# Performance work log

Measured on AMD Instinct MI355X. Metric: run time of the kernel, lower is better.

The kernel has to match this reference:

```python
import jax, jax.numpy as jnp
import numpy as np

# Llama-3-8B-style attention config (from init_kwargs)
DIM = 4096
N_HEADS = 32
N_KV_HEADS = 8
HEAD_DIM = DIM // N_HEADS          # 128
N_REP = N_HEADS // N_KV_HEADS      # 4 (GQA replication)
ROPE_THETA = 10000.0
W_SCALE = 0.02


def setup_inputs() -> dict:
    key = jax.random.key(0)
    kx, kq, kk, kv, ko = jax.random.split(key, 5)
    bsz, seqlen = 1, 2048
    x = jax.random.normal(kx, (bsz, seqlen, DIM), dtype=jnp.float32)
    # nn.Linear(in, out, bias=False) -> store as [in, out] so y = x @ W
    wq = jax.random.normal(kq, (DIM, N_HEADS * HEAD_DIM), dtype=jnp.float32) * W_SCALE
    wk = jax.random.normal(kk, (DIM, N_KV_HEADS * HEAD_DIM), dtype=jnp.float32) * W_SCALE
    wv = jax.random.normal(kv, (DIM, N_KV_HEADS * HEAD_DIM), dtype=jnp.float32) * W_SCALE
    wo = jax.random.normal(ko, (N_HEADS * HEAD_DIM, DIM), dtype=jnp.float32) * W_SCALE
    return {"x": x, "wq": wq, "wk": wk, "wv": wv, "wo": wo, "start_pos": 0}


def _rope_cos_sin(seqlen: int):
    # precompute_freqs_cis: freqs[j] = theta^(-2j/dim), angles = outer(t, freqs)
    inv_freq = 1.0 / (ROPE_THETA ** (jnp.arange(0, HEAD_DIM, 2, dtype=jnp.float32) / HEAD_DIM))
    angles = jnp.arange(seqlen, dtype=jnp.float32)[:, None] * inv_freq[None, :]  # [s, hd/2]
    return jnp.cos(angles), jnp.sin(angles)


def _apply_rope(t, cos, sin):
    # t: [b, s, h, hd]; pairs (even, odd) form complex numbers, rotate by angle
    tr, ti = t[..., 0::2], t[..., 1::2]
    c = cos[None, :, None, :]
    s = sin[None, :, None, :]
    out = jnp.stack([tr * c - ti * s, tr * s + ti * c], axis=-1)  # [b,s,h,hd/2,2]
    return out.reshape(t.shape)


def reference(x, wq, wk, wv, wo, start_pos):
    bsz, seqlen, _ = x.shape
    xq = (x @ wq).reshape(bsz, seqlen, N_HEADS, HEAD_DIM)
    xk = (x @ wk).reshape(bsz, seqlen, N_KV_HEADS, HEAD_DIM)
    xv = (x @ wv).reshape(bsz, seqlen, N_KV_HEADS, HEAD_DIM)

    cos, sin = _rope_cos_sin(seqlen)
    xq = _apply_rope(xq, cos, sin)
    xk = _apply_rope(xk, cos, sin)

    # GQA: repeat_interleave KV heads to match query heads
    xk = jnp.repeat(xk, N_REP, axis=2)
    xv = jnp.repeat(xv, N_REP, axis=2)

    scale = 1.0 / jnp.sqrt(jnp.float32(HEAD_DIM))
    scores = jnp.einsum('bqhd,bkhd->bhqk', xq, xk) * scale  # [b,h,s,s]
    causal = jnp.tril(jnp.ones((seqlen, seqlen), dtype=bool))
    scores = jnp.where(causal[None, None], scores, -jnp.inf)
    probs = jax.nn.softmax(scores, axis=-1)

    out = jnp.einsum('bhqk,bkhd->bqhd', probs, xv)
    out = out.reshape(bsz, seqlen, N_HEADS * HEAD_DIM)
    return out @ wo
```

## Files before the change

kernel.cpp:

```cpp
#include <hip/hip_runtime.h>
#include <stdint.h>

typedef __attribute__((ext_vector_type(8))) short bf16x8;
typedef __attribute__((ext_vector_type(4))) short bf16x4;
typedef __attribute__((ext_vector_type(4))) float f32x4;
typedef __attribute__((ext_vector_type(4))) unsigned short u16x4;

#define DIM   4096
#define SEQ   2048
#define NH    32
#define NKV   8
#define HD    128
#define QKV_N 6144
#define ATT_SCALE 0.08838834764831845f

static __device__ __forceinline__ unsigned short f2bf_bits(float f) {
  uint32_t x = __builtin_bit_cast(uint32_t, f);
  x += 0x7fffu + ((x >> 16) & 1u);
  return (unsigned short)(x >> 16);
}
static __device__ __forceinline__ float bf_bits2f(unsigned short u) {
  uint32_t x = ((uint32_t)u) << 16;
  return __builtin_bit_cast(float, x);
}

__global__ __launch_bounds__(256) void transpose_f32_bf16(
    const float* __restrict__ in, unsigned short* __restrict__ out,
    int ld_in, int ld_out) {
  __shared__ unsigned short sh[32][33];
  const int c0 = blockIdx.x * 32, r0 = blockIdx.y * 32;
  const int t = threadIdx.x;
  const int cc = t & 31, rr = (t >> 5) * 4;
#pragma unroll
  for (int p = 0; p < 4; ++p)
    sh[cc][rr + p] = f2bf_bits(in[(size_t)(r0 + rr + p) * ld_in + (c0 + cc)]);
  __syncthreads();
#pragma unroll
  for (int p = 0; p < 4; ++p)
    out[(size_t)(c0 + rr + p) * ld_out + (r0 + cc)] = sh[rr + p][cc];
}

__global__ __launch_bounds__(256) void transpose_bf16(
    const unsigned short* __restrict__ in, unsigned short* __restrict__ out,
    int ld_in, int ld_out) {
  __shared__ unsigned short sh[32][33];
  const int c0 = blockIdx.x * 32, r0 = blockIdx.y * 32;
  const int t = threadIdx.x;
  const int cc = t & 31, rr = (t >> 5) * 4;
#pragma unroll
  for (int p = 0; p < 4; ++p)
    sh[cc][rr + p] = in[(size_t)(r0 + rr + p) * ld_in + (c0 + cc)];
  __syncthreads();
#pragma unroll
  for (int p = 0; p < 4; ++p)
    out[(size_t)(c0 + rr + p) * ld_out + (r0 + cc)] = sh[rr + p][cc];
}

__global__ __launch_bounds__(256) void convert_f32_bf16(
    const float* __restrict__ in, unsigned short* __restrict__ out) {
  const int i = (blockIdx.x * 256 + threadIdx.x) * 4;
  const float4 v = *(const float4*)&in[i];
  u16x4 w;
  w[0] = f2bf_bits(v.x); w[1] = f2bf_bits(v.y);
  w[2] = f2bf_bits(v.z); w[3] = f2bf_bits(v.w);
  *(u16x4*)&out[i] = w;
}

#define BM 128
#define BN 128
#define BK 32
#define LDSS 40

template <bool OUT_FP32>
__global__ __launch_bounds__(256) void gemm_bt(
    const unsigned short* __restrict__ A, int lda,
    const unsigned short* __restrict__ Bt, int ldb,
    void* __restrict__ C_, int ldc, int K) {
  __shared__ __align__(16) unsigned short ldsA[BM * LDSS];
  __shared__ __align__(16) unsigned short ldsB[BN * LDSS];
  const int t = threadIdx.x;
  const int wave = t >> 6, lane = t & 63;
  const int lane16 = lane & 15, quad = lane >> 4;
  const int m0 = blockIdx.y * BM, n0 = blockIdx.x * BN;
  const int wrow = (wave >> 1) * 64, wcol = (wave & 1) * 64;

  f32x4 acc[4][4];
#pragma unroll
  for (int i = 0; i < 4; ++i)
#pragma unroll
    for (int j = 0; j < 4; ++j) acc[i][j] = (f32x4){0.f, 0.f, 0.f, 0.f};

  const int sr = t >> 2;
  const int sc = (t & 3) * 8;

  for (int kk = 0; kk < K; kk += BK) {
    __syncthreads();
#pragma unroll
    for (int i = 0; i < 2; ++i) {
      const int r = sr + i * 64;
      *(bf16x8*)&ldsA[r * LDSS + sc] =
          *(const bf16x8*)&A[(size_t)(m0 + r) * lda + kk + sc];
      *(bf16x8*)&ldsB[r * LDSS + sc] =
          *(const bf16x8*)&Bt[(size_t)(n0 + r) * ldb + kk + sc];
    }
    __syncthreads();

    bf16x8 af[4], bfr[4];
#pragma unroll
    for (int mi = 0; mi < 4; ++mi)
      af[mi] = *(const bf16x8*)&ldsA[(wrow + mi * 16 + lane16) * LDSS + quad * 8];
#pragma unroll
    for (int ni = 0; ni < 4; ++ni)
      bfr[ni] = *(const bf16x8*)&ldsB[(wcol + ni * 16 + lane16) * LDSS + quad * 8];
#pragma unroll
    for (int mi = 0; mi < 4; ++mi)
#pragma unroll
      for (int ni = 0; ni < 4; ++ni)
        acc[mi][ni] = __builtin_amdgcn_mfma_f32_16x16x32_bf16(
            af[mi], bfr[ni], acc[mi][ni], 0, 0, 0);
  }

#pragma unroll
  for (int mi = 0; mi < 4; ++mi)
#pragma unroll
    for (int ni = 0; ni < 4; ++ni)
#pragma unroll
      for (int r = 0; r < 4; ++r) {
        const int row = m0 + wrow + mi * 16 + quad * 4 + r;
        const int col = n0 + wcol + ni * 16 + lane16;
        if (OUT_FP32)
          ((float*)C_)[(size_t)row * ldc + col] = acc[mi][ni][r];
        else
          ((unsigned short*)C_)[(size_t)row * ldc + col] = f2bf_bits(acc[mi][ni][r]);
      }
}

__global__ __launch_bounds__(256) void rope_kernel(unsigned short* __restrict__ qkv) {
  const int idx = blockIdx.x * 256 + threadIdx.x;
  const int pos = idx / 2560;
  const int rem = idx - pos * 2560;
  const int head = rem >> 6;
  const int i = rem & 63;
  const float inv_freq = __expf(-(float)(2 * i) * (9.210340371976184f / 128.0f));
  const float ang = (float)pos * inv_freq;
  float s, c;
  __sincosf(ang, &s, &c);
  const int col = (head < 32) ? head * 128 + 2 * i
                              : 4096 + (head - 32) * 128 + 2 * i;
  unsigned short* p = qkv + (size_t)pos * QKV_N + col;
  const float tr = bf_bits2f(p[0]), ti = bf_bits2f(p[1]);
  p[0] = f2bf_bits(tr * c - ti * s);
  p[1] = f2bf_bits(tr * s + ti * c);
}

#define QT 64
#define KT 64
#define KLS (HD + 8)
#define VLS (KT + 8)

__global__ __launch_bounds__(256) void attn_kernel(
    const unsigned short* __restrict__ qkv,
    const unsigned short* __restrict__ vT,
    unsigned short* __restrict__ attn) {
  __shared__ __align__(16) unsigned short kls[KT][KLS];
  __shared__ __align__(16) unsigned short vls[HD][VLS];

  const int t = threadIdx.x;
  const int wave = t >> 6, lane = t & 63;
  const int lane16 = lane & 15, quad = lane >> 4;
  const int h = blockIdx.y, kvh = h >> 2;
  const int qt = (gridDim.x - 1) - blockIdx.x;
  const int q0 = qt * QT;
  const int wq0 = q0 + wave * 16;
  const int qrow = wq0 + lane16;

  const unsigned short* qbase = qkv + (size_t)wq0 * QKV_N + h * HD;
  const unsigned short* kbase = qkv + 4096 + kvh * HD;
  const unsigned short* vbase = vT + (size_t)kvh * HD * SEQ;

  bf16x8 qf[4];
#pragma unroll
  for (int dc = 0; dc < 4; ++dc)
    qf[dc] = *(const bf16x8*)&qbase[(size_t)lane16 * QKV_N + dc * 32 + quad * 8];

  f32x4 o[8];
#pragma unroll
  for (int i = 0; i < 8; ++i) o[i] = (f32x4){0.f, 0.f, 0.f, 0.f};
  float m = -INFINITY, l = 0.f;

  const int nkb = qt + 1;
  for (int kb = 0; kb < nkb; ++kb) {
    const int key0 = kb * KT;
    __syncthreads();
    {
      const int r = t >> 2, c = (t & 3) * 8;
      const unsigned short* src = &kbase[(size_t)(key0 + r) * QKV_N];
#pragma unroll
      for (int j = 0; j < 4; ++j)
        *(bf16x8*)&kls[r][c + j * 32] = *(const bf16x8*)&src[c + j * 32];
    }
    {
      const int d = t >> 1, s0 = (t & 1) * 32;
      const unsigned short* src = &vbase[(size_t)d * SEQ + key0];
#pragma unroll
      for (int j = 0; j < 4; ++j)
        *(bf16x8*)&vls[d][s0 + j * 8] = *(const bf16x8*)&src[s0 + j * 8];
    }
    __syncthreads();

    f32x4 S[4];
#pragma unroll
    for (int kt = 0; kt < 4; ++kt) {
      f32x4 sacc = (f32x4){0.f, 0.f, 0.f, 0.f};
#pragma unroll
      for (int dc = 0; dc < 4; ++dc) {
        const bf16x8 kf = *(const bf16x8*)&kls[kt * 16 + lane16][dc * 32 + quad * 8];
        sacc = __builtin_amdgcn_mfma_f32_16x16x32_bf16(kf, qf[dc], sacc, 0, 0, 0);
      }
      S[kt] = sacc;
    }

    float sv[4][4], mx = -INFINITY;
#pragma unroll
    for (int kt = 0; kt < 4; ++kt)
#pragma unroll
      for (int r = 0; r < 4; ++r) {
        const int key = key0 + kt * 16 + quad * 4 + r;
        sv[kt][r] = (key <= qrow) ? S[kt][r] * ATT_SCALE : -INFINITY;
        mx = fmaxf(mx, sv[kt][r]);
      }
    mx = fmaxf(mx, __shfl_xor(mx, 16, 64));
    mx = fmaxf(mx, __shfl_xor(mx, 32, 64));
    const float newm = fmaxf(m, mx);
    const float alpha = __expf(m - newm);
    m = newm;
    float p[4][4], rs = 0.f;
#pragma unroll
    for (int kt = 0; kt < 4; ++kt)
#pragma unroll
      for (int r = 0; r < 4; ++r) {
        p[kt][r] = __expf(sv[kt][r] - newm);
        rs += p[kt][r];
      }
    rs += __shfl_xor(rs, 16, 64);
    rs += __shfl_xor(rs, 32, 64);
    l = l * alpha + rs;
#pragma unroll
    for (int dt = 0; dt < 8; ++dt)
#pragma unroll
      for (int r = 0; r < 4; ++r) o[dt][r] *= alpha;

    bf16x4 pb[4];
#pragma unroll
    for (int kt = 0; kt < 4; ++kt) {
      bf16x4 w;
      w[0] = (short)f2bf_bits(p[kt][0]); w[1] = (short)f2bf_bits(p[kt][1]);
      w[2] = (short)f2bf_bits(p[kt][2]); w[3] = (short)f2bf_bits(p[kt][3]);
      pb[kt] = w;
    }

#pragma unroll
    for (int dt = 0; dt < 8; ++dt)
#pragma unroll
      for (int kt = 0; kt < 4; ++kt) {
        const bf16x4 vf = *(const bf16x4*)&vls[dt * 16 + lane16][kt * 16 + quad * 4];
        o[dt] = __builtin_amdgcn_mfma_f32_16x16x16bf16_1k(vf, pb[kt], o[dt], 0, 0, 0);
      }
  }

  const float inv_l = 1.0f / l;
  unsigned short* dst = attn + (size_t)qrow * DIM + h * HD;
#pragma unroll
  for (int dt = 0; dt < 8; ++dt) {
    u16x4 w;
#pragma unroll
    for (int r = 0; r < 4; ++r) w[r] = f2bf_bits(o[dt][r] * inv_l);
    *(u16x4*)&dst[dt * 16 + quad * 4] = w;
  }
}

extern "C" void kernel_launch(void* const* d_in, const int* in_sizes, int n_in,
                              void* d_out, int out_size, void* d_ws, size_t ws_size,
                              hipStream_t stream) {
  const float* x  = (const float*)d_in[0];
  const float* wq = (const float*)d_in[1];
  const float* wk = (const float*)d_in[2];
  const float* wv = (const float*)d_in[3];
  const float* wo = (const float*)d_in[4];
  float* out = (float*)d_out;

  unsigned short* wqkvT = (unsigned short*)d_ws;
  unsigned short* woT   = wqkvT;
  unsigned short* qkv   = wqkvT + (size_t)6144 * 4096;
  unsigned short* vT    = qkv   + (size_t)2048 * 6144;
  unsigned short* attn  = vT    + (size_t)1024 * 2048;
  unsigned short* xb    = attn;

  const dim3 b256(256);
  transpose_f32_bf16<<<dim3(128, 128), b256, 0, stream>>>(wq, wqkvT, 4096, 4096);
  transpose_f32_bf16<<<dim3(32, 128),  b256, 0, stream>>>(wk, wqkvT + (size_t)4096 * 4096, 1024, 4096);
  transpose_f32_bf16<<<dim3(32, 128),  b256, 0, stream>>>(wv, wqkvT + (size_t)5120 * 4096, 1024, 4096);
  convert_f32_bf16<<<dim3(SEQ * DIM / 1024), b256, 0, stream>>>(x, xb);

  gemm_bt<false><<<dim3(QKV_N / BN, SEQ / BM), b256, 0, stream>>>(
      xb, DIM, wqkvT, DIM, qkv, QKV_N, DIM);

  rope_kernel<<<dim3((SEQ * 2560) / 256), b256, 0, stream>>>(qkv);

  transpose_bf16<<<dim3(32, 64), b256, 0, stream>>>(qkv + 5120, vT, 6144, 2048);

  attn_kernel<<<dim3(SEQ / QT, NH), b256, 0, stream>>>(qkv, vT, attn);

  transpose_f32_bf16<<<dim3(128, 128), b256, 0, stream>>>(wo, woT, 4096, 4096);

  gemm_bt<true><<<dim3(DIM / BN, SEQ / BM), b256, 0, stream>>>(
      attn, DIM, woT, DIM, out, DIM, DIM);
}
```

Before: 616.3 us.

## Use direct global-to-LDS loads in GEMM and pipeline, pair, and swizzle attention

The GEMM now stages A and B tiles with global_load_lds straight into unpadded LDS, skipping the register round trip. The attention kernel handles two query tiles per block, pairing a long causal tile with a short one to even out work, and halves the grid. It also prefetches the next K/V tile into registers during compute, XOR-swizzles the V LDS layout in place of padding, and raises wave priority around the MFMAs. A lazy-rescale threshold skips updating the running max and rescaling the accumulators unless the block max exceeds the current max by more than a margin, which trades some exponent headroom for fewer rescales. The unpadded GEMM LDS layout may cause bank conflicts.

New measurement: 540.4 us. -12.3%, faster.

```diff
diff --git a/kernel.cpp b/kernel.cpp
--- a/kernel.cpp
+++ b/kernel.cpp
@@ -22,6 +22,13 @@
 static __device__ __forceinline__ float bf_bits2f(unsigned short u) {
   uint32_t x = ((uint32_t)u) << 16;
   return __builtin_bit_cast(float, x);
+}
+
+static __device__ __forceinline__ void g2l16(const unsigned short* gp,
+                                             unsigned short* lp) {
+  __builtin_amdgcn_global_load_lds(
+      (const __attribute__((address_space(1))) unsigned int*)gp,
+      (__attribute__((address_space(3))) unsigned int*)lp, 16, 0, 0);
 }
 
 __global__ __launch_bounds__(256) void transpose_f32_bf16(
@@ -69,15 +76,14 @@
 #define BM 128
 #define BN 128
 #define BK 32
-#define LDSS 40
 
 template <bool OUT_FP32>
 __global__ __launch_bounds__(256) void gemm_bt(
     const unsigned short* __restrict__ A, int lda,
     const unsigned short* __restrict__ Bt, int ldb,
     void* __restrict__ C_, int ldc, int K) {
-  __shared__ __align__(16) unsigned short ldsA[BM * LDSS];
-  __shared__ __align__(16) unsigned short ldsB[BN * LDSS];
+  __shared__ __align__(16) unsigned short ldsA[BM * BK];
+  __shared__ __align__(16) unsigned short ldsB[BN * BK];
   const int t = threadIdx.x;
   const int wave = t >> 6, lane = t & 63;
   const int lane16 = lane & 15, quad = lane >> 4;
@@ -90,28 +96,28 @@
 #pragma unroll
     for (int j = 0; j < 4; ++j) acc[i][j] = (f32x4){0.f, 0.f, 0.f, 0.f};
 
-  const int sr = t >> 2;
-  const int sc = (t & 3) * 8;
+  const int srow = t >> 2;
+  const int scol = (t & 3) * 8;
+  const size_t arow0 = (size_t)(m0 + srow) * lda;
+  const size_t arow1 = (size_t)(m0 + 64 + srow) * lda;
+  const size_t brow0 = (size_t)(n0 + srow) * ldb;
+  const size_t brow1 = (size_t)(n0 + 64 + srow) * ldb;
 
   for (int kk = 0; kk < K; kk += BK) {
     __syncthreads();
-#pragma unroll
-    for (int i = 0; i < 2; ++i) {
-      const int r = sr + i * 64;
-      *(bf16x8*)&ldsA[r * LDSS + sc] =
-          *(const bf16x8*)&A[(size_t)(m0 + r) * lda + kk + sc];
-      *(bf16x8*)&ldsB[r * LDSS + sc] =
-          *(const bf16x8*)&Bt[(size_t)(n0 + r) * ldb + kk + sc];
-    }
+    g2l16(&A[arow0 + kk + scol],  &ldsA[t * 8]);
+    g2l16(&A[arow1 + kk + scol],  &ldsA[2048 + t * 8]);
+    g2l16(&Bt[brow0 + kk + scol], &ldsB[t * 8]);
+    g2l16(&Bt[brow1 + kk + scol], &ldsB[2048 + t * 8]);
     __syncthreads();
 
     bf16x8 af[4], bfr[4];
 #pragma unroll
     for (int mi = 0; mi < 4; ++mi)
-      af[mi] = *(const bf16x8*)&ldsA[(wrow + mi * 16 + lane16) * LDSS + quad * 8];
+      af[mi] = *(const bf16x8*)&ldsA[(wrow + mi * 16 + lane16) * BK + quad * 8];
 #pragma unroll
     for (int ni = 0; ni < 4; ++ni)
-      bfr[ni] = *(const bf16x8*)&ldsB[(wcol + ni * 16 + lane16) * LDSS + quad * 8];
+      bfr[ni] = *(const bf16x8*)&ldsB[(wcol + ni * 16 + lane16) * BK + quad * 8];
 #pragma unroll
     for (int mi = 0; mi < 4; ++mi)
 #pragma unroll
@@ -156,126 +162,163 @@
 #define QT 64
 #define KT 64
 #define KLS (HD + 8)
-#define VLS (KT + 8)
+#define NQ  (SEQ / QT)
+#define DEFER_THR 8.0f
 
 __global__ __launch_bounds__(256) void attn_kernel(
     const unsigned short* __restrict__ qkv,
     const unsigned short* __restrict__ vT,
     unsigned short* __restrict__ attn) {
   __shared__ __align__(16) unsigned short kls[KT][KLS];
-  __shared__ __align__(16) unsigned short vls[HD][VLS];
+  __shared__ __align__(16) unsigned short vls[HD][KT];
 
   const int t = threadIdx.x;
   const int wave = t >> 6, lane = t & 63;
   const int lane16 = lane & 15, quad = lane >> 4;
   const int h = blockIdx.y, kvh = h >> 2;
-  const int qt = (gridDim.x - 1) - blockIdx.x;
-  const int q0 = qt * QT;
-  const int wq0 = q0 + wave * 16;
-  const int qrow = wq0 + lane16;
-
-  const unsigned short* qbase = qkv + (size_t)wq0 * QKV_N + h * HD;
   const unsigned short* kbase = qkv + 4096 + kvh * HD;
   const unsigned short* vbase = vT + (size_t)kvh * HD * SEQ;
 
-  bf16x8 qf[4];
-#pragma unroll
-  for (int dc = 0; dc < 4; ++dc)
-    qf[dc] = *(const bf16x8*)&qbase[(size_t)lane16 * QKV_N + dc * 32 + quad * 8];
-
-  f32x4 o[8];
-#pragma unroll
-  for (int i = 0; i < 8; ++i) o[i] = (f32x4){0.f, 0.f, 0.f, 0.f};
-  float m = -INFINITY, l = 0.f;
-
-  const int nkb = qt + 1;
-  for (int kb = 0; kb < nkb; ++kb) {
-    const int key0 = kb * KT;
-    __syncthreads();
-    {
-      const int r = t >> 2, c = (t & 3) * 8;
-      const unsigned short* src = &kbase[(size_t)(key0 + r) * QKV_N];
+  const int kr = t >> 2, kc = (t & 3) * 8;
+  const int vd = t >> 1;
+  const int vu0 = (t & 1) * 8;
+  const int vswz = (vd & 7) << 1;
+  const int rswz = (lane16 & 7) << 1;
+  const unsigned short* ksrc0 = &kbase[(size_t)kr * QKV_N + kc];
+  const unsigned short* vsrc0 = &vbase[(size_t)vd * SEQ + (t & 1) * 32];
+
+  bf16x8 kreg[4], vreg[4];
+
+  for (int half = 0; half < 2; ++half) {
+    const int qt = half ? (int)blockIdx.x : (NQ - 1 - (int)blockIdx.x);
+    const int q0 = qt * QT;
+    const int wq0 = q0 + wave * 16;
+    const int qrow = wq0 + lane16;
+    const int nkb = qt + 1;
+
+#pragma unroll
+    for (int j = 0; j < 4; ++j) kreg[j] = *(const bf16x8*)&ksrc0[j * 32];
+#pragma unroll
+    for (int j = 0; j < 4; ++j) vreg[j] = *(const bf16x8*)&vsrc0[j * 8];
+
+    const unsigned short* qbase = qkv + (size_t)wq0 * QKV_N + h * HD;
+
+    bf16x8 qf[4];
+#pragma unroll
+    for (int dc = 0; dc < 4; ++dc)
+      qf[dc] = *(const bf16x8*)&qbase[(size_t)lane16 * QKV_N + dc * 32 + quad * 8];
+
+    f32x4 o[8];
+#pragma unroll
+    for (int i = 0; i < 8; ++i) o[i] = (f32x4){0.f, 0.f, 0.f, 0.f};
+    float m = -INFINITY, l = 0.f;
+
+    for (int kb = 0; kb < nkb; ++kb) {
+      const int key0 = kb * KT;
+      __syncthreads();
+
 #pragma unroll
       for (int j = 0; j < 4; ++j)
-        *(bf16x8*)&kls[r][c + j * 32] = *(const bf16x8*)&src[c + j * 32];
+        *(bf16x8*)&kls[kr][kc + j * 32] = kreg[j];
+#pragma unroll
+      for (int j = 0; j < 4; ++j)
+        *(bf16x8*)&vls[vd][((vu0 + j * 2) ^ vswz) * 4] = vreg[j];
+
+      if (kb + 1 < nkb) {
+        const unsigned short* ks = ksrc0 + (size_t)(kb + 1) * KT * QKV_N;
+        const unsigned short* vs = vsrc0 + (kb + 1) * KT;
+#pragma unroll
+        for (int j = 0; j < 4; ++j) kreg[j] = *(const bf16x8*)&ks[j * 32];
+#pragma unroll
+        for (int j = 0; j < 4; ++j) vreg[j] = *(const bf16x8*)&vs[j * 8];
+      }
+
+      asm volatile("s_waitcnt lgkmcnt(0)" ::: "memory");
+      __builtin_amdgcn_s_barrier();
+
+      f32x4 S[4];
+      __builtin_amdgcn_s_setprio(1);
+#pragma unroll
+      for (int kt = 0; kt < 4; ++kt) {
+        f32x4 sacc = (f32x4){0.f, 0.f, 0.f, 0.f};
+#pragma unroll
+        for (int dc = 0; dc < 4; ++dc) {
+          const bf16x8 kf = *(const bf16x8*)&kls[kt * 16 + lane16][dc * 32 + quad * 8];
+          sacc = __builtin_amdgcn_mfma_f32_16x16x32_bf16(kf, qf[dc], sacc, 0, 0, 0);
+        }
+        S[kt] = sacc;
+      }
+      __builtin_amdgcn_s_setprio(0);
+
+      float sv[4][4], mx = -INFINITY;
+#pragma unroll
+      for (int kt = 0; kt < 4; ++kt)
+#pragma unroll
+        for (int r = 0; r < 4; ++r) {
+          const int key = key0 + kt * 16 + quad * 4 + r;
+          sv[kt][r] = (key <= qrow) ? S[kt][r] * ATT_SCALE : -INFINITY;
+          mx = fmaxf(mx, sv[kt][r]);
+        }
+      mx = fmaxf(mx, __shfl_xor(mx, 16, 64));
+      mx = fmaxf(mx, __shfl_xor(mx, 32, 64));
+
+      const bool skip = __all(mx <= m + DEFER_THR);
+      float alpha = 1.f;
+      if (!skip) {
+        const float newm = fmaxf(m, mx);
+        alpha = __expf(m - newm);
+        m = newm;
+      }
+      float p[4][4], rs = 0.f;
+#pragma unroll
+      for (int kt = 0; kt < 4; ++kt)
+#pragma unroll
+        for (int r = 0; r < 4; ++r) {
+          p[kt][r] = __expf(sv[kt][r] - m);
+          rs += p[kt][r];
+        }
+      rs += __shfl_xor(rs, 16, 64);
+      rs += __shfl_xor(rs, 32, 64);
+      if (skip) {
+        l += rs;
+      } else {
+        l = l * alpha + rs;
+#pragma unroll
+        for (int dt = 0; dt < 8; ++dt)
+#pragma unroll
+          for (int r = 0; r < 4; ++r) o[dt][r] *= alpha;
+      }
+
+      bf16x4 pb[4];
+#pragma unroll
+      for (int kt = 0; kt < 4; ++kt) {
+        bf16x4 w;
+        w[0] = (short)f2bf_bits(p[kt][0]); w[1] = (short)f2bf_bits(p[kt][1]);
+        w[2] = (short)f2bf_bits(p[kt][2]); w[3] = (short)f2bf_bits(p[kt][3]);
+        pb[kt] = w;
+      }
+
+      __builtin_amdgcn_s_setprio(1);
+#pragma unroll
+      for (int dt = 0; dt < 8; ++dt)
+#pragma unroll
+        for (int kt = 0; kt < 4; ++kt) {
+          const bf16x4 vf = *(const bf16x4*)
+              &vls[dt * 16 + lane16][(((kt * 4 + quad) ^ rswz)) * 4];
+          o[dt] = __builtin_amdgcn_mfma_f32_16x16x16bf16_1k(vf, pb[kt], o[dt], 0, 0, 0);
+        }
+      __builtin_amdgcn_s_setprio(0);
     }
-    {
-      const int d = t >> 1, s0 = (t & 1) * 32;
-      const unsigned short* src = &vbase[(size_t)d * SEQ + key0];
-#pragma unroll
-      for (int j = 0; j < 4; ++j)
-        *(bf16x8*)&vls[d][s0 + j * 8] = *(const bf16x8*)&src[s0 + j * 8];
+
+    const float inv_l = 1.0f / l;
+    unsigned short* dst = attn + (size_t)qrow * DIM + h * HD;
+#pragma unroll
+    for (int dt = 0; dt < 8; ++dt) {
+      u16x4 w;
+#pragma unroll
+      for (int r = 0; r < 4; ++r) w[r] = f2bf_bits(o[dt][r] * inv_l);
+      *(u16x4*)&dst[dt * 16 + quad * 4] = w;
     }
-    __syncthreads();
-
-    f32x4 S[4];
-#pragma unroll
-    for (int kt = 0; kt < 4; ++kt) {
-      f32x4 sacc = (f32x4){0.f, 0.f, 0.f, 0.f};
-#pragma unroll
-      for (int dc = 0; dc < 4; ++dc) {
-        const bf16x8 kf = *(const bf16x8*)&kls[kt * 16 + lane16][dc * 32 + quad * 8];
-        sacc = __builtin_amdgcn_mfma_f32_16x16x32_bf16(kf, qf[dc], sacc, 0, 0, 0);
-      }
-      S[kt] = sacc;
-    }
-
-    float sv[4][4], mx = -INFINITY;
-#pragma unroll
-    for (int kt = 0; kt < 4; ++kt)
-#pragma unroll
-      for (int r = 0; r < 4; ++r) {
-        const int key = key0 + kt * 16 + quad * 4 + r;
-        sv[kt][r] = (key <= qrow) ? S[kt][r] * ATT_SCALE : -INFINITY;
-        mx = fmaxf(mx, sv[kt][r]);
-      }
-    mx = fmaxf(mx, __shfl_xor(mx, 16, 64));
-    mx = fmaxf(mx, __shfl_xor(mx, 32, 64));
-    const float newm = fmaxf(m, mx);
-    const float alpha = __expf(m - newm);
-    m = newm;
-    float p[4][4], rs = 0.f;
-#pragma unroll
-    for (int kt = 0; kt < 4; ++kt)
-#pragma unroll
-      for (int r = 0; r < 4; ++r) {
-        p[kt][r] = __expf(sv[kt][r] - newm);
-        rs += p[kt][r];
-      }
-    rs += __shfl_xor(rs, 16, 64);
-    rs += __shfl_xor(rs, 32, 64);
-    l = l * alpha + rs;
-#pragma unroll
-    for (int dt = 0; dt < 8; ++dt)
-#pragma unroll
-      for (int r = 0; r < 4; ++r) o[dt][r] *= alpha;
-
-    bf16x4 pb[4];
-#pragma unroll
-    for (int kt = 0; kt < 4; ++kt) {
-      bf16x4 w;
-      w[0] = (short)f2bf_bits(p[kt][0]); w[1] = (short)f2bf_bits(p[kt][1]);
-      w[2] = (short)f2bf_bits(p[kt][2]); w[3] = (short)f2bf_bits(p[kt][3]);
-      pb[kt] = w;
-    }
-
-#pragma unroll
-    for (int dt = 0; dt < 8; ++dt)
-#pragma unroll
-      for (int kt = 0; kt < 4; ++kt) {
-        const bf16x4 vf = *(const bf16x4*)&vls[dt * 16 + lane16][kt * 16 + quad * 4];
-        o[dt] = __builtin_amdgcn_mfma_f32_16x16x16bf16_1k(vf, pb[kt], o[dt], 0, 0, 0);
-      }
-  }
-
-  const float inv_l = 1.0f / l;
-  unsigned short* dst = attn + (size_t)qrow * DIM + h * HD;
-#pragma unroll
-  for (int dt = 0; dt < 8; ++dt) {
-    u16x4 w;
-#pragma unroll
-    for (int r = 0; r < 4; ++r) w[r] = f2bf_bits(o[dt][r] * inv_l);
-    *(u16x4*)&dst[dt * 16 + quad * 4] = w;
   }
 }
 
@@ -309,7 +352,7 @@
 
   transpose_bf16<<<dim3(32, 64), b256, 0, stream>>>(qkv + 5120, vT, 6144, 2048);
 
-  attn_kernel<<<dim3(SEQ / QT, NH), b256, 0, stream>>>(qkv, vT, attn);
+  attn_kernel<<<dim3(NQ / 2, NH), b256, 0, stream>>>(qkv, vT, attn);
 
   transpose_f32_bf16<<<dim3(128, 128), b256, 0, stream>>>(wo, woT, 4096, 4096);
 
```
